# Performance work log

Hardware: AMD Instinct MI355X
Metric: run time of the kernel (lower is better)

The kernel has to match this reference:

```python
import jax, jax.numpy as jnp
import numpy as np

N, E, F, H, G = 50000, 800000, 64, 64, 100

def setup_inputs() -> dict:
    key = jax.random.key(0)
    ks = jax.random.split(key, 12)
    x = jax.random.normal(ks[0], (N, F), dtype=jnp.float32)
    edge_index = jax.random.randint(ks[1], (2, E), 0, N, dtype=jnp.int64)
    batch = jnp.sort(jax.random.randint(ks[2], (N,), 0, G, dtype=jnp.int64))
    s1 = 1.0 / np.sqrt(F); s2 = 1.0 / np.sqrt(H)
    W1 = jax.random.normal(ks[3], (2, F, H), dtype=jnp.float32) * s1
    b1 = jnp.zeros((H,), dtype=jnp.float32)
    W2 = jax.random.normal(ks[4], (2, H, H), dtype=jnp.float32) * s2
    b2 = jnp.zeros((H,), dtype=jnp.float32)
    gamma = jnp.ones((H,), dtype=jnp.float32)
    beta = jnp.zeros((H,), dtype=jnp.float32)
    linW = jax.random.normal(ks[5], (H, 1), dtype=jnp.float32) * s2
    linb = jnp.zeros((1,), dtype=jnp.float32)
    return {"x": x, "edge_index": edge_index, "batch": batch, "W1": W1, "b1": b1,
            "W2": W2, "b2": b2, "gamma": gamma, "beta": beta, "linW": linW, "linb": linb}

def _edge_norm(row, col, n):
    # get_laplacian(sym) + lambda_max=2: Lhat off-diag weight = -d_i^{-1/2} d_j^{-1/2}, diag = 0
    deg = jax.ops.segment_sum(jnp.ones(row.shape[0], jnp.float32), row, num_segments=n)
    dis = jnp.where(deg > 0, deg ** -0.5, 0.0)
    return -dis[row] * dis[col]

def _cheb(x, row, col, w, W, b):
    # K=2: out = T0(Lhat)x @ W0 + T1(Lhat)x @ W1 + b, T1 = Lhat x via scatter-add
    Tx1 = jax.ops.segment_sum(w[:, None] * x[row], col, num_segments=x.shape[0])
    return x @ W[0] + Tx1 @ W[1] + b

def reference(x, edge_index, batch, W1, b1, W2, b2, gamma, beta, linW, linb):
    row, col = edge_index[0], edge_index[1]
    n = x.shape[0]
    w = _edge_norm(row, col, n)
    h = _cheb(x, row, col, w, W1, b1)
    # BatchNorm1d (training-mode batch stats, eps=1e-5)
    mu = jnp.mean(h, axis=0)
    var = jnp.var(h, axis=0)
    h = (h - mu) * jax.lax.rsqrt(var + 1e-5) * gamma + beta
    # LeakyReLU (default slope 0.01)
    h = jnp.where(h >= 0, h, 0.01 * h)
    h = _cheb(h, row, col, w, W2, b2)
    # global_mean_pool over graph ids
    sums = jax.ops.segment_sum(h, batch, num_segments=G)
    cnts = jax.ops.segment_sum(jnp.ones(n, jnp.float32), batch, num_segments=G)
    pooled = sums / jnp.maximum(cnts, 1.0)[:, None]
    # dropout: identity (eval)
    return pooled @ linW + linb
```

## Files before the change

kernel.cpp:

```cpp
#include <hip/hip_runtime.h>

#define HDIM 64
#define BH 64
#define HNODES 25600
#define HBINS 12800
#define SBINS 12544
#define GR 32


__device__ __forceinline__ int lbound(const int* __restrict__ b, int n, int v) {
    int lo = 0, hi = n;
    while (lo < hi) { int m = (lo + hi) >> 1; if (b[m] < v) lo = m + 1; else hi = m; }
    return lo;
}


__global__ __launch_bounds__(256) void k_histP(const int* __restrict__ row,
                                               const int* __restrict__ col,
                                               unsigned short* __restrict__ cntP,
                                               unsigned short* __restrict__ degP,
                                               int E, int N, int slice) {
    __shared__ unsigned hbin[HBINS];
    int blk   = blockIdx.x;
    int phase = blockIdx.y & 1;
    int isRow = blockIdx.y >> 1;
    const int* keys = isRow ? row : col;
    unsigned short* outP = isRow ? degP : cntP;
    int lo = phase * HNODES;
    int spanN = min(HNODES, N - lo);
    int binsU = (spanN + 1) >> 1;
    for (int i = threadIdx.x; i < binsU; i += 256) hbin[i] = 0;
    __syncthreads();
    int e0 = blk * slice, e1 = min(e0 + slice, E);
    for (int e = e0 + threadIdx.x; e < e1; e += 256) {
        int c = keys[e] - lo;
        if ((unsigned)c < (unsigned)spanN)
            atomicAdd(&hbin[c >> 1], 1u << ((c & 1) << 4));
    }
    __syncthreads();
    unsigned* outU = (unsigned*)(outP + (size_t)blk * N + lo);
    for (int i = threadIdx.x; i < binsU; i += 256) outU[i] = hbin[i];
}

__global__ void k_prefA(unsigned short* __restrict__ cntP,
                        const unsigned short* __restrict__ degP,
                        int* __restrict__ cnt, float* __restrict__ dis, int N) {
    int i = blockIdx.x * blockDim.x + threadIdx.x;
    if (i >= N) return;
    int run = 0;
    #pragma unroll 8
    for (int b = 0; b < BH; ++b) {
        int v = cntP[(size_t)b * N + i];
        cntP[(size_t)b * N + i] = (unsigned short)run;
        run += v;
    }
    cnt[i] = run;
    int d = 0;
    #pragma unroll 8
    for (int b = 0; b < BH; ++b) d += degP[(size_t)b * N + i];
    dis[i] = d > 0 ? rsqrtf((float)d) : 0.0f;
}

__global__ __launch_bounds__(1024) void k_scan1(const int* __restrict__ cnt,
                                                int* __restrict__ start,
                                                int* __restrict__ bsum, int n) {
    __shared__ int wsum[16];
    int i = blockIdx.x * 1024 + threadIdx.x;
    int lane = threadIdx.x & 63, w = threadIdx.x >> 6;
    int v = (i < n) ? cnt[i] : 0;
    int incl = v;
    #pragma unroll
    for (int off = 1; off < 64; off <<= 1) {
        int u = __shfl_up(incl, off, 64);
        if (lane >= off) incl += u;
    }
    if (lane == 63) wsum[w] = incl;
    __syncthreads();
    if (w == 0) {
        int s = (lane < 16) ? wsum[lane] : 0;
        int si = s;
        #pragma unroll
        for (int off = 1; off < 16; off <<= 1) {
            int u = __shfl_up(si, off, 64);
            if (lane >= off) si += u;
        }
        if (lane < 16) wsum[lane] = si - s;
    }
    __syncthreads();
    int excl = incl - v + wsum[w];
    if (i < n) start[i] = excl;
    if (threadIdx.x == 1023) bsum[blockIdx.x] = excl + v;
}

__global__ void k_scan2(int* __restrict__ bsum, int nb) {
    int lane = threadIdx.x;
    if (lane >= 64) return;
    int v = (lane < nb) ? bsum[lane] : 0;
    int incl = v;
    #pragma unroll
    for (int off = 1; off < 64; off <<= 1) {
        int u = __shfl_up(incl, off, 64);
        if (lane >= off) incl += u;
    }
    if (lane < nb) bsum[lane] = incl - v;
}

__global__ void k_scan3(int* __restrict__ start, const int* __restrict__ bsum, int n) {
    int i = blockIdx.x * blockDim.x + threadIdx.x;
    if (i < n) start[i] += bsum[i >> 10];
}

__global__ __launch_bounds__(256) void k_sortfill(const int* __restrict__ row,
                                                  const int* __restrict__ col,
                                                  const unsigned short* __restrict__ cntP,
                                                  const int* __restrict__ start,
                                                  int* __restrict__ er,
                                                  int E, int N, int slice) {
    __shared__ int cur[SBINS];
    int blk = blockIdx.x;
    int lo = blockIdx.y * SBINS;
    int span = min(SBINS, N - lo);
    for (int i = threadIdx.x; i < span; i += 256)
        cur[i] = start[lo + i] + (int)cntP[(size_t)blk * N + lo + i];
    __syncthreads();
    int e0 = blk * slice, e1 = min(e0 + slice, E);
    for (int e = e0 + threadIdx.x; e < e1; e += 256) {
        int c = col[e] - lo;
        int rv = row[e];
        if ((unsigned)c < (unsigned)span) {
            int pos = atomicAdd(&cur[c], 1);
            er[pos] = rv;
        }
    }
}


__global__ __launch_bounds__(256) void k_gather1(const int* __restrict__ er,
                                                 const int* __restrict__ start,
                                                 const int* __restrict__ cnt,
                                                 const float* __restrict__ dis,
                                                 const float* __restrict__ x,
                                                 float* __restrict__ Tx, int n) {
    int i = blockIdx.x * 4 + (threadIdx.x >> 6);
    if (i >= n) return;
    int lane = threadIdx.x & 63;
    int q = lane >> 4;
    int s4 = (lane & 15) * 4;
    int s = start[i], nd = cnt[i];
    float di = dis[i];
    float4 acc = make_float4(0.f, 0.f, 0.f, 0.f);
    int k = q;
    for (; k + 4 < nd; k += 8) {
        int r0 = er[s + k], r1 = er[s + k + 4];
        float w0 = -dis[r0] * di, w1 = -dis[r1] * di;
        float4 v0 = *reinterpret_cast<const float4*>(&x[(size_t)r0 * HDIM + s4]);
        float4 v1 = *reinterpret_cast<const float4*>(&x[(size_t)r1 * HDIM + s4]);
        acc.x = fmaf(w0, v0.x, acc.x); acc.y = fmaf(w0, v0.y, acc.y);
        acc.z = fmaf(w0, v0.z, acc.z); acc.w = fmaf(w0, v0.w, acc.w);
        acc.x = fmaf(w1, v1.x, acc.x); acc.y = fmaf(w1, v1.y, acc.y);
        acc.z = fmaf(w1, v1.z, acc.z); acc.w = fmaf(w1, v1.w, acc.w);
    }
    if (k < nd) {
        int r0 = er[s + k];
        float w0 = -dis[r0] * di;
        float4 v0 = *reinterpret_cast<const float4*>(&x[(size_t)r0 * HDIM + s4]);
        acc.x = fmaf(w0, v0.x, acc.x); acc.y = fmaf(w0, v0.y, acc.y);
        acc.z = fmaf(w0, v0.z, acc.z); acc.w = fmaf(w0, v0.w, acc.w);
    }
    #pragma unroll
    for (int off = 16; off <= 32; off <<= 1) {
        acc.x += __shfl_xor(acc.x, off, 64);
        acc.y += __shfl_xor(acc.y, off, 64);
        acc.z += __shfl_xor(acc.z, off, 64);
        acc.w += __shfl_xor(acc.w, off, 64);
    }
    if (q == 0) *reinterpret_cast<float4*>(&Tx[(size_t)i * HDIM + s4]) = acc;
}

__global__ __launch_bounds__(512) void k_gemm1(const float* __restrict__ x,
                                               float* __restrict__ TxH,
                                               const float* __restrict__ W1,
                                               const float* __restrict__ b1,
                                               float* __restrict__ pstat, int n) {
    __shared__ float xs[GR][HDIM];
    __shared__ float ts[GR][HDIM];
    __shared__ float pl[GR][HDIM];
    int tid  = threadIdx.x;
    int j    = tid & 63;
    int half = (tid >> 6) & 1;
    int w2   = tid >> 7;
    int base = blockIdx.x * GR;

    const float* Wb = W1 + (half ? HDIM * HDIM : 0);
    float4 wr[16];
    #pragma unroll
    for (int k4 = 0; k4 < 16; ++k4) {
        wr[k4].x = Wb[(k4 * 4 + 0) * HDIM + j];
        wr[k4].y = Wb[(k4 * 4 + 1) * HDIM + j];
        wr[k4].z = Wb[(k4 * 4 + 2) * HDIM + j];
        wr[k4].w = Wb[(k4 * 4 + 3) * HDIM + j];
    }
    float bj = b1[j];

    {
        int v = tid;
        int r = base + (v >> 4);
        int rc = min(r, n - 1);
        int c = (v & 15) * 4;
        ((float4*)xs)[v] = *(const float4*)&x[(size_t)rc * HDIM + c];
        ((float4*)ts)[v] = *(const float4*)&TxH[(size_t)rc * HDIM + c];
    }
    __syncthreads();

    const float(*src)[HDIM] = half ? ts : xs;
    float acc[8];
    #pragma unroll
    for (int m = 0; m < 8; ++m) {
        int lr = w2 * 8 + m;
        const float4* rp = (const float4*)src[lr];
        float a = 0.f;
        #pragma unroll
        for (int k4 = 0; k4 < 16; ++k4) {
            float4 v = rp[k4];
            a = fmaf(v.x, wr[k4].x, a);
            a = fmaf(v.y, wr[k4].y, a);
            a = fmaf(v.z, wr[k4].z, a);
            a = fmaf(v.w, wr[k4].w, a);
        }
        acc[m] = a;
    }

    if (half == 1) {
        #pragma unroll
        for (int m = 0; m < 8; ++m) pl[w2 * 8 + m][j] = acc[m];
    }
    __syncthreads();

    float sacc = 0.f, ssacc = 0.f;
    if (half == 0) {
        #pragma unroll
        for (int m = 0; m < 8; ++m) {
            int lr = w2 * 8 + m;
            int r = base + lr;
            if (r < n) {
                float tot = acc[m] + pl[lr][j] + bj;
                TxH[(size_t)r * HDIM + j] = tot;
                sacc += tot;
                ssacc = fmaf(tot, tot, ssacc);
            }
        }
    }
    __syncthreads();
    if (half == 0) {
        pl[w2][j]     = sacc;
        pl[4 + w2][j] = ssacc;
    }
    __syncthreads();
    if (half == 0 && w2 == 0) {
        float s  = pl[0][j] + pl[1][j] + pl[2][j] + pl[3][j];
        float ss = pl[4][j] + pl[5][j] + pl[6][j] + pl[7][j];
        pstat[(size_t)blockIdx.x * 128 + j]      = s;
        pstat[(size_t)blockIdx.x * 128 + 64 + j] = ss;
    }
}

__global__ __launch_bounds__(256) void k_statred(const float* __restrict__ pstat,
                                                 float* __restrict__ stats, int nb) {
    int idx = blockIdx.x;
    float s = 0.f;
    for (int b = threadIdx.x; b < nb; b += 256)
        s += pstat[(size_t)b * 128 + idx];
    __shared__ float red[256];
    red[threadIdx.x] = s;
    __syncthreads();
    for (int off = 128; off > 0; off >>= 1) {
        if (threadIdx.x < off) red[threadIdx.x] += red[threadIdx.x + off];
        __syncthreads();
    }
    if (threadIdx.x == 0) stats[idx] = red[0];
}

__global__ void k_prep(const float* __restrict__ stats,
                       const float* __restrict__ gamma, const float* __restrict__ beta,
                       const float* __restrict__ W2, const float* __restrict__ b2,
                       const float* __restrict__ linW, const float* __restrict__ linb,
                       float* __restrict__ scale, float* __restrict__ shift,
                       float* __restrict__ u0, float* __restrict__ u1,
                       float* __restrict__ c0, int n) {
    int k = threadIdx.x;
    if (k >= HDIM) return;
    float inv_n = 1.0f / (float)n;
    float mu  = stats[k] * inv_n;
    float var = stats[64 + k] * inv_n - mu * mu;
    float rs  = rsqrtf(var + 1e-5f);
    float sc  = rs * gamma[k];
    scale[k] = sc;
    shift[k] = beta[k] - mu * sc;
    float a0 = 0.f, a1 = 0.f;
    #pragma unroll 8
    for (int j = 0; j < HDIM; ++j) {
        float lw = linW[j];
        a0 = fmaf(W2[k * HDIM + j], lw, a0);
        a1 = fmaf(W2[HDIM * HDIM + k * HDIM + j], lw, a1);
    }
    u0[k] = a0;
    u1[k] = a1;
    if (k == 0) {
        float c = linb[0];
        for (int j = 0; j < HDIM; ++j) c = fmaf(b2[j], linW[j], c);
        c0[0] = c;
    }
}

__global__ __launch_bounds__(256) void k_node(const float* __restrict__ h,
                                              const float* __restrict__ scale,
                                              const float* __restrict__ shift,
                                              const float* __restrict__ u0,
                                              const float* __restrict__ u1,
                                              float* __restrict__ a, float* __restrict__ t,
                                              int n) {
    int i = blockIdx.x * 4 + (threadIdx.x >> 6);
    if (i >= n) return;
    int j = threadIdx.x & 63;
    float v = fmaf(h[(size_t)i * HDIM + j], scale[j], shift[j]);
    v = v >= 0.f ? v : 0.01f * v;
    float p0 = v * u0[j];
    float p1 = v * u1[j];
    #pragma unroll
    for (int off = 32; off > 0; off >>= 1) {
        p0 += __shfl_xor(p0, off, 64);
        p1 += __shfl_xor(p1, off, 64);
    }
    if (j == 0) { a[i] = p0; t[i] = p1; }
}

__global__ void k_gather2(const int* __restrict__ er, const int* __restrict__ start,
                          const int* __restrict__ cnt, const float* __restrict__ dis,
                          const float* __restrict__ t, const float* __restrict__ a,
                          float* __restrict__ s2, int n) {
    int i = blockIdx.x * blockDim.x + threadIdx.x;
    if (i >= n) return;
    int s = start[i], nd = cnt[i];
    float di = dis[i];
    float acc = a[i];
    int k = 0;
    for (; k + 1 < nd; k += 2) {
        int r0 = er[s + k], r1 = er[s + k + 1];
        float v0 = -dis[r0] * di * t[r0];
        float v1 = -dis[r1] * di * t[r1];
        acc += v0 + v1;
    }
    if (k < nd) {
        int r0 = er[s + k];
        acc = fmaf(-dis[r0] * di, t[r0], acc);
    }
    s2[i] = acc;
}

__global__ __launch_bounds__(256) void k_pool2(const float* __restrict__ s2,
                                               const int* __restrict__ batch,
                                               const float* __restrict__ c0,
                                               const float* __restrict__ linb,
                                               float* __restrict__ out, int n) {
    int g = blockIdx.x;
    int lo = lbound(batch, n, g);
    int hi = lbound(batch, n, g + 1);
    float s = 0.f;
    for (int i = lo + threadIdx.x; i < hi; i += 256) s += s2[i];
    __shared__ float red[256];
    red[threadIdx.x] = s;
    __syncthreads();
    for (int off = 128; off > 0; off >>= 1) {
        if (threadIdx.x < off) red[threadIdx.x] += red[threadIdx.x + off];
        __syncthreads();
    }
    if (threadIdx.x == 0) {
        int cntg = hi - lo;
        out[g] = cntg > 0 ? red[0] / (float)cntg + c0[0] : linb[0];
    }
}


extern "C" void kernel_launch(void* const* d_in, const int* in_sizes, int n_in,
                              void* d_out, int out_size, void* d_ws, size_t ws_size,
                              hipStream_t stream) {
    const float* x     = (const float*)d_in[0];
    const int*   eidx  = (const int*)d_in[1];
    const int*   batch = (const int*)d_in[2];
    const float* W1    = (const float*)d_in[3];
    const float* b1    = (const float*)d_in[4];
    const float* W2    = (const float*)d_in[5];
    const float* b2    = (const float*)d_in[6];
    const float* gamma = (const float*)d_in[7];
    const float* beta  = (const float*)d_in[8];
    const float* linW  = (const float*)d_in[9];
    const float* linb  = (const float*)d_in[10];
    float* out = (float*)d_out;

    const int N = in_sizes[0] / HDIM;
    const int E = in_sizes[1] / 2;
    const int G = out_size;
    const int NB = (N + 1023) / 1024;
    const int slice = (E + BH - 1) / BH;
    const int NGB = (N + GR - 1) / GR;

    const int* row = eidx;
    const int* col = eidx + E;

    char* wsb = (char*)d_ws;
    float* TxH  = (float*)wsb;               wsb += (size_t)N * HDIM * 4;
    unsigned short* cntP = (unsigned short*)TxH;
    unsigned short* degP = cntP + (size_t)BH * N;
    int*   cnt   = (int*)wsb;                wsb += (size_t)N * 4;
    int*   start = (int*)wsb;                wsb += (size_t)N * 4;
    int*   bsum  = (int*)wsb;                wsb += (size_t)NB * 4 + 64;
    int*   er    = (int*)wsb;                wsb += (size_t)E * 4;
    float* dis   = (float*)wsb;              wsb += (size_t)N * 4;
    float* a     = (float*)wsb;              wsb += (size_t)N * 4;
    float* t     = (float*)wsb;              wsb += (size_t)N * 4;
    float* s2    = (float*)wsb;              wsb += (size_t)N * 4;
    float* pstat = (float*)wsb;              wsb += (size_t)NGB * 128 * 4;
    float* stats = (float*)wsb;              wsb += 128 * 4;
    float* scale = (float*)wsb;              wsb += HDIM * 4;
    float* shift = (float*)wsb;              wsb += HDIM * 4;
    float* u0    = (float*)wsb;              wsb += HDIM * 4;
    float* u1    = (float*)wsb;              wsb += HDIM * 4;
    float* c0    = (float*)wsb;              wsb += 64;

    k_histP<<<dim3(BH, 4), 256, 0, stream>>>(row, col, cntP, degP, E, N, slice);
    k_prefA<<<(N + 255) / 256, 256, 0, stream>>>(cntP, degP, cnt, dis, N);
    k_scan1<<<NB, 1024, 0, stream>>>(cnt, start, bsum, N);
    k_scan2<<<1, 64, 0, stream>>>(bsum, NB);
    k_scan3<<<(N + 255) / 256, 256, 0, stream>>>(start, bsum, N);
    k_sortfill<<<dim3(BH, 4), 256, 0, stream>>>(row, col, cntP, start, er, E, N, slice);
    k_gather1<<<(N + 3) / 4, 256, 0, stream>>>(er, start, cnt, dis, x, TxH, N);
    k_gemm1<<<NGB, 512, 0, stream>>>(x, TxH, W1, b1, pstat, N);
    k_statred<<<128, 256, 0, stream>>>(pstat, stats, NGB);
    k_prep<<<1, 64, 0, stream>>>(stats, gamma, beta, W2, b2, linW, linb,
                                 scale, shift, u0, u1, c0, N);
    k_node<<<(N + 3) / 4, 256, 0, stream>>>(TxH, scale, shift, u0, u1, a, t, N);
    k_gather2<<<(N + 255) / 256, 256, 0, stream>>>(er, start, cnt, dis, t, a, s2, N);
    k_pool2<<<G, 256, 0, stream>>>(s2, batch, c0, linb, out, N);
}
```

Measured before the change: 169.0 us.

## Apply W1 before aggregation and fold source degree scaling into node features

Reorders the first Chebyshev layer so the dense GEMM runs first: z = x@W0 + b and y = dis * (x@W1). A gather kernel then sums y over in-neighbours, scales by the destination degree factor, and also emits the BatchNorm partial statistics. The second-layer scalar gather likewise premultiplies t by dis, which removes per-edge dis lookups and multiplies from both gathers. The cost is two extra N×64 intermediate buffers (z and y) written and read back, and a statistics reduction over many more per-block partials.

```diff
diff --git a/kernel.cpp b/kernel.cpp
--- a/kernel.cpp
+++ b/kernel.cpp
@@ -135,56 +135,13 @@
 }
 
 
-__global__ __launch_bounds__(256) void k_gather1(const int* __restrict__ er,
-                                                 const int* __restrict__ start,
-                                                 const int* __restrict__ cnt,
-                                                 const float* __restrict__ dis,
-                                                 const float* __restrict__ x,
-                                                 float* __restrict__ Tx, int n) {
-    int i = blockIdx.x * 4 + (threadIdx.x >> 6);
-    if (i >= n) return;
-    int lane = threadIdx.x & 63;
-    int q = lane >> 4;
-    int s4 = (lane & 15) * 4;
-    int s = start[i], nd = cnt[i];
-    float di = dis[i];
-    float4 acc = make_float4(0.f, 0.f, 0.f, 0.f);
-    int k = q;
-    for (; k + 4 < nd; k += 8) {
-        int r0 = er[s + k], r1 = er[s + k + 4];
-        float w0 = -dis[r0] * di, w1 = -dis[r1] * di;
-        float4 v0 = *reinterpret_cast<const float4*>(&x[(size_t)r0 * HDIM + s4]);
-        float4 v1 = *reinterpret_cast<const float4*>(&x[(size_t)r1 * HDIM + s4]);
-        acc.x = fmaf(w0, v0.x, acc.x); acc.y = fmaf(w0, v0.y, acc.y);
-        acc.z = fmaf(w0, v0.z, acc.z); acc.w = fmaf(w0, v0.w, acc.w);
-        acc.x = fmaf(w1, v1.x, acc.x); acc.y = fmaf(w1, v1.y, acc.y);
-        acc.z = fmaf(w1, v1.z, acc.z); acc.w = fmaf(w1, v1.w, acc.w);
-    }
-    if (k < nd) {
-        int r0 = er[s + k];
-        float w0 = -dis[r0] * di;
-        float4 v0 = *reinterpret_cast<const float4*>(&x[(size_t)r0 * HDIM + s4]);
-        acc.x = fmaf(w0, v0.x, acc.x); acc.y = fmaf(w0, v0.y, acc.y);
-        acc.z = fmaf(w0, v0.z, acc.z); acc.w = fmaf(w0, v0.w, acc.w);
-    }
-    #pragma unroll
-    for (int off = 16; off <= 32; off <<= 1) {
-        acc.x += __shfl_xor(acc.x, off, 64);
-        acc.y += __shfl_xor(acc.y, off, 64);
-        acc.z += __shfl_xor(acc.z, off, 64);
-        acc.w += __shfl_xor(acc.w, off, 64);
-    }
-    if (q == 0) *reinterpret_cast<float4*>(&Tx[(size_t)i * HDIM + s4]) = acc;
-}
-
-__global__ __launch_bounds__(512) void k_gemm1(const float* __restrict__ x,
-                                               float* __restrict__ TxH,
+__global__ __launch_bounds__(512) void k_gemm2(const float* __restrict__ x,
+                                               const float* __restrict__ dis,
                                                const float* __restrict__ W1,
                                                const float* __restrict__ b1,
-                                               float* __restrict__ pstat, int n) {
+                                               float* __restrict__ z,
+                                               float* __restrict__ y, int n) {
     __shared__ float xs[GR][HDIM];
-    __shared__ float ts[GR][HDIM];
-    __shared__ float pl[GR][HDIM];
     int tid  = threadIdx.x;
     int j    = tid & 63;
     int half = (tid >> 6) & 1;
@@ -208,57 +165,66 @@
         int rc = min(r, n - 1);
         int c = (v & 15) * 4;
         ((float4*)xs)[v] = *(const float4*)&x[(size_t)rc * HDIM + c];
-        ((float4*)ts)[v] = *(const float4*)&TxH[(size_t)rc * HDIM + c];
-    }
-    __syncthreads();
-
-    const float(*src)[HDIM] = half ? ts : xs;
-    float acc[8];
+    }
+    __syncthreads();
+
     #pragma unroll
     for (int m = 0; m < 8; ++m) {
         int lr = w2 * 8 + m;
-        const float4* rp = (const float4*)src[lr];
-        float a = 0.f;
-        #pragma unroll
-        for (int k4 = 0; k4 < 16; ++k4) {
-            float4 v = rp[k4];
-            a = fmaf(v.x, wr[k4].x, a);
-            a = fmaf(v.y, wr[k4].y, a);
-            a = fmaf(v.z, wr[k4].z, a);
-            a = fmaf(v.w, wr[k4].w, a);
+        int r = base + lr;
+        if (r < n) {
+            const float4* rp = (const float4*)xs[lr];
+            float a = 0.f;
+            #pragma unroll
+            for (int k4 = 0; k4 < 16; ++k4) {
+                float4 v = rp[k4];
+                a = fmaf(v.x, wr[k4].x, a);
+                a = fmaf(v.y, wr[k4].y, a);
+                a = fmaf(v.z, wr[k4].z, a);
+                a = fmaf(v.w, wr[k4].w, a);
+            }
+            if (half == 0) z[(size_t)r * HDIM + j] = a + bj;
+            else           y[(size_t)r * HDIM + j] = dis[r] * a;
         }
-        acc[m] = a;
-    }
-
-    if (half == 1) {
-        #pragma unroll
-        for (int m = 0; m < 8; ++m) pl[w2 * 8 + m][j] = acc[m];
-    }
-    __syncthreads();
-
-    float sacc = 0.f, ssacc = 0.f;
-    if (half == 0) {
-        #pragma unroll
-        for (int m = 0; m < 8; ++m) {
-            int lr = w2 * 8 + m;
-            int r = base + lr;
-            if (r < n) {
-                float tot = acc[m] + pl[lr][j] + bj;
-                TxH[(size_t)r * HDIM + j] = tot;
-                sacc += tot;
-                ssacc = fmaf(tot, tot, ssacc);
-            }
+    }
+}
+
+__global__ __launch_bounds__(256) void k_gatherH(const int* __restrict__ er,
+                                                 const int* __restrict__ start,
+                                                 const int* __restrict__ cnt,
+                                                 const float* __restrict__ dis,
+                                                 const float* __restrict__ y,
+                                                 const float* __restrict__ z,
+                                                 float* __restrict__ h,
+                                                 float* __restrict__ pstat, int n) {
+    __shared__ float red[2][4][HDIM];
+    int w = threadIdx.x >> 6;
+    int j = threadIdx.x & 63;
+    int i = blockIdx.x * 4 + w;
+    float hv = 0.f;
+    if (i < n) {
+        int s = start[i], nd = cnt[i];
+        float di = dis[i];
+        float a0 = 0.f, a1 = 0.f, a2 = 0.f, a3 = 0.f;
+        int k = 0;
+        for (; k + 3 < nd; k += 4) {
+            int r0 = er[s + k], r1 = er[s + k + 1];
+            int r2 = er[s + k + 2], r3 = er[s + k + 3];
+            a0 += y[(size_t)r0 * HDIM + j];
+            a1 += y[(size_t)r1 * HDIM + j];
+            a2 += y[(size_t)r2 * HDIM + j];
+            a3 += y[(size_t)r3 * HDIM + j];
         }
-    }
-    __syncthreads();
-    if (half == 0) {
-        pl[w2][j]     = sacc;
-        pl[4 + w2][j] = ssacc;
-    }
-    __syncthreads();
-    if (half == 0 && w2 == 0) {
-        float s  = pl[0][j] + pl[1][j] + pl[2][j] + pl[3][j];
-        float ss = pl[4][j] + pl[5][j] + pl[6][j] + pl[7][j];
+        for (; k < nd; ++k) a0 += y[(size_t)er[s + k] * HDIM + j];
+        hv = z[(size_t)i * HDIM + j] - di * ((a0 + a1) + (a2 + a3));
+        h[(size_t)i * HDIM + j] = hv;
+    }
+    red[0][w][j] = hv;
+    red[1][w][j] = hv * hv;
+    __syncthreads();
+    if (w == 0) {
+        float s  = red[0][0][j] + red[0][1][j] + red[0][2][j] + red[0][3][j];
+        float ss = red[1][0][j] + red[1][1][j] + red[1][2][j] + red[1][3][j];
         pstat[(size_t)blockIdx.x * 128 + j]      = s;
         pstat[(size_t)blockIdx.x * 128 + 64 + j] = ss;
     }
@@ -317,6 +283,7 @@
                                               const float* __restrict__ shift,
                                               const float* __restrict__ u0,
                                               const float* __restrict__ u1,
+                                              const float* __restrict__ dis,
                                               float* __restrict__ a, float* __restrict__ t,
                                               int n) {
     int i = blockIdx.x * 4 + (threadIdx.x >> 6);
@@ -331,7 +298,7 @@
         p0 += __shfl_xor(p0, off, 64);
         p1 += __shfl_xor(p1, off, 64);
     }
-    if (j == 0) { a[i] = p0; t[i] = p1; }
+    if (j == 0) { a[i] = p0; t[i] = dis[i] * p1; }
 }
 
 __global__ void k_gather2(const int* __restrict__ er, const int* __restrict__ start,
@@ -341,20 +308,16 @@
     int i = blockIdx.x * blockDim.x + threadIdx.x;
     if (i >= n) return;
     int s = start[i], nd = cnt[i];
-    float di = dis[i];
-    float acc = a[i];
+    float s0 = 0.f, s1 = 0.f, s2v = 0.f, s3 = 0.f;
     int k = 0;
-    for (; k + 1 < nd; k += 2) {
-        int r0 = er[s + k], r1 = er[s + k + 1];
-        float v0 = -dis[r0] * di * t[r0];
-        float v1 = -dis[r1] * di * t[r1];
-        acc += v0 + v1;
-    }
-    if (k < nd) {
-        int r0 = er[s + k];
-        acc = fmaf(-dis[r0] * di, t[r0], acc);
-    }
-    s2[i] = acc;
+    for (; k + 3 < nd; k += 4) {
+        s0 += t[er[s + k]];
+        s1 += t[er[s + k + 1]];
+        s2v += t[er[s + k + 2]];
+        s3 += t[er[s + k + 3]];
+    }
+    for (; k < nd; ++k) s0 += t[er[s + k]];
+    s2[i] = a[i] - dis[i] * ((s0 + s1) + (s2v + s3));
 }
 
 __global__ __launch_bounds__(256) void k_pool2(const float* __restrict__ s2,
@@ -402,15 +365,17 @@
     const int G = out_size;
     const int NB = (N + 1023) / 1024;
     const int slice = (E + BH - 1) / BH;
-    const int NGB = (N + GR - 1) / GR;
+    const int NHB = (N + 3) / 4;
 
     const int* row = eidx;
     const int* col = eidx + E;
 
     char* wsb = (char*)d_ws;
-    float* TxH  = (float*)wsb;               wsb += (size_t)N * HDIM * 4;
-    unsigned short* cntP = (unsigned short*)TxH;
+    float* h    = (float*)wsb;               wsb += (size_t)N * HDIM * 4;
+    unsigned short* cntP = (unsigned short*)h;
     unsigned short* degP = cntP + (size_t)BH * N;
+    float* z    = (float*)wsb;               wsb += (size_t)N * HDIM * 4;
+    float* y    = (float*)wsb;               wsb += (size_t)N * HDIM * 4;
     int*   cnt   = (int*)wsb;                wsb += (size_t)N * 4;
     int*   start = (int*)wsb;                wsb += (size_t)N * 4;
     int*   bsum  = (int*)wsb;                wsb += (size_t)NB * 4 + 64;
@@ -419,7 +384,7 @@
     float* a     = (float*)wsb;              wsb += (size_t)N * 4;
     float* t     = (float*)wsb;              wsb += (size_t)N * 4;
     float* s2    = (float*)wsb;              wsb += (size_t)N * 4;
-    float* pstat = (float*)wsb;              wsb += (size_t)NGB * 128 * 4;
+    float* pstat = (float*)wsb;              wsb += (size_t)NHB * 128 * 4;
     float* stats = (float*)wsb;              wsb += 128 * 4;
     float* scale = (float*)wsb;              wsb += HDIM * 4;
     float* shift = (float*)wsb;              wsb += HDIM * 4;
@@ -433,12 +398,12 @@
     k_scan2<<<1, 64, 0, stream>>>(bsum, NB);
     k_scan3<<<(N + 255) / 256, 256, 0, stream>>>(start, bsum, N);
     k_sortfill<<<dim3(BH, 4), 256, 0, stream>>>(row, col, cntP, start, er, E, N, slice);
-    k_gather1<<<(N + 3) / 4, 256, 0, stream>>>(er, start, cnt, dis, x, TxH, N);
-    k_gemm1<<<NGB, 512, 0, stream>>>(x, TxH, W1, b1, pstat, N);
-    k_statred<<<128, 256, 0, stream>>>(pstat, stats, NGB);
+    k_gemm2<<<(N + GR - 1) / GR, 512, 0, stream>>>(x, dis, W1, b1, z, y, N);
+    k_gatherH<<<NHB, 256, 0, stream>>>(er, start, cnt, dis, y, z, h, pstat, N);
+    k_statred<<<128, 256, 0, stream>>>(pstat, stats, NHB);
     k_prep<<<1, 64, 0, stream>>>(stats, gamma, beta, W2, b2, linW, linb,
                                  scale, shift, u0, u1, c0, N);
-    k_node<<<(N + 3) / 4, 256, 0, stream>>>(TxH, scale, shift, u0, u1, a, t, N);
+    k_node<<<(N + 3) / 4, 256, 0, stream>>>(h, scale, shift, u0, u1, dis, a, t, N);
     k_gather2<<<(N + 255) / 256, 256, 0, stream>>>(er, start, cnt, dis, t, a, s2, N);
     k_pool2<<<G, 256, 0, stream>>>(s2, batch, c0, linb, out, N);
 }
```

Result: slower. 195.5 us (+15.7%).
